# Performance work log

Hardware: AMD Instinct MI355X
Metric: run time of the kernel (lower is better)

## Reference

```python
import jax, jax.numpy as jnp
import numpy as np

L = 248      # max_clip_seq_len
WIN = 3      # window_size
H = 8        # attention heads
D = 768      # input/output dim
HID = 256    # rope hidden dim
SIGMA = 2.0
EPS_LN = 1e-5


def _layernorm(x, g, b):
    m = jnp.mean(x, axis=-1, keepdims=True)
    v = jnp.var(x, axis=-1, keepdims=True)
    return (x - m) / jnp.sqrt(v + EPS_LN) * g + b


def _normalize(x):
    n = jnp.linalg.norm(x, axis=-1, keepdims=True)
    return x / jnp.maximum(n, 1e-12)


def _peb_forward(word_feat, text_feat_full, word_pos, ctx_W, ctx_b, in_W, in_b,
                 out_W, out_b, cn_g, cn_b, r1_W, r1_b, ln_g, ln_b, r2_W, r2_b,
                 pos_emb, pos_temp):
    B, N, _ = word_feat.shape
    valid = word_pos != -1                              # [B,N] bool
    vf = valid.astype(word_feat.dtype)[..., None]       # [B,N,1]
    wp = jnp.clip(word_pos, 0, L - 1)                   # [B,N]
    half = WIN // 2
    offs = jnp.arange(-half, half + 1)
    positions = jnp.clip(wp[..., None] + offs[None, None, :], 0, L - 1)
    ctx = text_feat_full[jnp.arange(B)[:, None, None], positions]
    ctx_anchor = (ctx.reshape(B, N, WIN * D) @ ctx_W + ctx_b) * vf       # [B,N,D]
    q = word_feat * vf                                  # word_proj is Identity (768->768)
    # MultiheadAttention (batch_first), query=q, key=value=ctx_anchor
    hd = D // H
    qp = (q @ in_W[:, :D] + in_b[:D]).reshape(B, N, H, hd)
    kp = (ctx_anchor @ in_W[:, D:2 * D] + in_b[D:2 * D]).reshape(B, N, H, hd)
    vp = (ctx_anchor @ in_W[:, 2 * D:] + in_b[2 * D:]).reshape(B, N, H, hd)
    scores = jnp.einsum('bqhd,bkhd->bhqk', qp, kp) / jnp.sqrt(jnp.asarray(hd, q.dtype))
    attn = jax.nn.softmax(scores, axis=-1)
    ao = jnp.einsum('bhqk,bkhd->bqhd', attn, vp).reshape(B, N, D)
    attn_out = ao @ out_W + out_b
    x = _layernorm(q + attn_out, cn_g, cn_b) * vf       # word_feat_with_ctx
    # rope_mapping: Linear -> GELU -> LayerNorm -> Linear
    rope = _layernorm(jax.nn.gelu(x @ r1_W + r1_b, approximate=False), ln_g, ln_b) @ r2_W + r2_b
    rope_n = _normalize(rope)
    clip_ref_n = _normalize(pos_emb)                    # [L,D]
    temp = jnp.maximum(pos_temp, 0.001)
    logits = jnp.einsum('bnd,ld->bnl', rope_n, clip_ref_n) / temp
    log_q = jax.nn.log_softmax(logits, axis=-1)
    # gaussian soft target over L positions
    pos_idx = jnp.arange(L, dtype=jnp.float32)
    d2 = (pos_idx[None, None, :] - wp[..., None].astype(jnp.float32)) ** 2
    targ = jnp.exp(-d2 / (2.0 * SIGMA ** 2))
    targ = targ / (targ.sum(axis=-1, keepdims=True) + 1e-12)
    lqv = log_q * vf
    tv = targ * vf
    n_valid = valid.sum().astype(jnp.float32)
    safe_t = jnp.where(tv > 0, tv, 1.0)
    kl = jnp.sum(jnp.where(tv > 0, tv * (jnp.log(safe_t) - lqv), 0.0)) / (n_valid + 1e-12)
    # relative position loss on cosine similarity
    pos_sim01 = (jnp.einsum('bnd,bmd->bnm', rope_n, rope_n) + 1.0) / 2.0
    wpf = wp.astype(jnp.float32)
    target_sim = 1.0 - jnp.abs(wpf[:, :, None] - wpf[:, None, :]) / float(L)
    vm2 = vf[:, :, 0][:, None, :] * vf[:, :, 0][:, :, None]
    rel = jnp.sum((pos_sim01 * vm2 - target_sim * vm2) ** 2) / (vm2.sum() + 1e-12)
    peb_loss = (1.0 * kl + 0.5 * rel) * 1.0             # kl_weight=1, rel_weight=0.5, peb_weight=1
    # scatter blended positional features to 248-length sequence (vectorized over batch)
    vals = 0.8 * pos_emb[wp] + 0.2 * rope               # [B,N,D]
    pos_s = jnp.where(valid, wp, L)                     # invalid -> OOB index, dropped
    emb = jnp.zeros((B, L, D), word_feat.dtype).at[jnp.arange(B)[:, None], pos_s].set(vals, mode='drop')
    return emb, peb_loss, kl, rel


def setup_inputs() -> dict:
    key = jax.random.key(0)
    ks = jax.random.split(key, 20)
    B, N = 128, 128
    word_feat = jax.random.normal(ks[0], (B, N, D), jnp.float32)
    text_feat_full = jax.random.normal(ks[1], (B, L, D), jnp.float32)
    # unique sorted positions per batch (scatter is then deterministic, matching torch)
    perms = jax.vmap(lambda k: jax.random.permutation(k, L))(jax.random.split(ks[2], B))
    word_pos = jnp.sort(perms[:, :N], axis=-1).astype(jnp.int32)
    s = 0.02
    return {
        'word_feat': word_feat,
        'text_feat_full': text_feat_full,
        'word_pos': word_pos,
        'ctx_W': s * jax.random.normal(ks[3], (WIN * D, D), jnp.float32),
        'ctx_b': s * jax.random.normal(ks[4], (D,), jnp.float32),
        'in_W': s * jax.random.normal(ks[5], (D, 3 * D), jnp.float32),
        'in_b': s * jax.random.normal(ks[6], (3 * D,), jnp.float32),
        'out_W': s * jax.random.normal(ks[7], (D, D), jnp.float32),
        'out_b': s * jax.random.normal(ks[8], (D,), jnp.float32),
        'cn_g': jnp.ones((D,), jnp.float32) + s * jax.random.normal(ks[9], (D,), jnp.float32),
        'cn_b': s * jax.random.normal(ks[10], (D,), jnp.float32),
        'r1_W': s * jax.random.normal(ks[11], (D, HID), jnp.float32),
        'r1_b': s * jax.random.normal(ks[12], (HID,), jnp.float32),
        'ln_g': jnp.ones((HID,), jnp.float32) + s * jax.random.normal(ks[13], (HID,), jnp.float32),
        'ln_b': s * jax.random.normal(ks[14], (HID,), jnp.float32),
        'r2_W': s * jax.random.normal(ks[15], (HID, D), jnp.float32),
        'r2_b': s * jax.random.normal(ks[16], (D,), jnp.float32),
        'pos_emb': jax.random.normal(ks[17], (L, D), jnp.float32),
        'pos_temp': jnp.asarray(1.0, jnp.float32),
    }


def reference(word_feat, text_feat_full, word_pos, ctx_W, ctx_b, in_W, in_b,
              out_W, out_b, cn_g, cn_b, r1_W, r1_b, ln_g, ln_b, r2_W, r2_b,
              pos_emb, pos_temp):
    return _peb_forward(word_feat, text_feat_full, word_pos, ctx_W, ctx_b, in_W, in_b,
                        out_W, out_b, cn_g, cn_b, r1_W, r1_b, ln_g, ln_b, r2_W, r2_b,
                        pos_emb, pos_temp)
```

## Files before the change

kernel.cpp:

```cpp
#include <hip/hip_runtime.h>
#include <math.h>

#define BB   128
#define NN   128
#define LL   248
#define DD   768
#define HH   8
#define HDh  96
#define HIDN 256
#define MROWS (BB*NN)
#define MB_   (1u<<20)
#define KVLD 1536

typedef unsigned short u16;
typedef unsigned int   u32;
typedef __attribute__((ext_vector_type(8))) short s16x8;
typedef __attribute__((ext_vector_type(4))) float f32x4;

__device__ __forceinline__ u16 f2bf(float x) {
    u32 u = __float_as_uint(x);
    u32 r = u + 0x7fffu + ((u >> 16) & 1u);
    return (u16)(r >> 16);
}
__device__ __forceinline__ float bf2f(u16 h) {
    return __uint_as_float(((u32)h) << 16);
}
__device__ __forceinline__ void gload16(const void* g, void* l) {
    __builtin_amdgcn_global_load_lds(
        (const __attribute__((address_space(1))) void*)g,
        (__attribute__((address_space(3))) void*)l, 16, 0, 0);
}

template<int NT>
__device__ __forceinline__ float breduce_sum(float v, float* red) {
    const int tid = threadIdx.x;
    red[tid] = v; __syncthreads();
#pragma unroll
    for (int o = NT / 2; o > 0; o >>= 1) {
        if (tid < o) red[tid] += red[tid + o];
        __syncthreads();
    }
    float r = red[0]; __syncthreads();
    return r;
}
__device__ __forceinline__ double breduce_sum_d256(double v, double* red) {
    const int tid = threadIdx.x;
    red[tid] = v; __syncthreads();
#pragma unroll
    for (int o = 128; o > 0; o >>= 1) {
        if (tid < o) red[tid] += red[tid + o];
        __syncthreads();
    }
    double r = red[0]; __syncthreads();
    return r;
}

#define TEXT_F4 (BB*LL*DD/4)
#define Q_F4    (MROWS*(DD/4))
__global__ __launch_bounds__(256)
void prep_all_kernel(const float* __restrict__ ctx_W, u16* __restrict__ ctx_Wt,
                     const float* __restrict__ in_W,  u16* __restrict__ in_Wt,
                     const float* __restrict__ out_W, u16* __restrict__ out_Wt,
                     const float* __restrict__ r1_W,  u16* __restrict__ r1_Wt,
                     const float* __restrict__ r2_W,  u16* __restrict__ r2_Wt,
                     const float* __restrict__ text,  u16* __restrict__ textb,
                     const float* __restrict__ wf,    u16* __restrict__ qb,
                     const int* __restrict__ wpos,    int* __restrict__ cpos,
                     const float* __restrict__ pe,    u16* __restrict__ clipb,
                     float* __restrict__ zbias) {
    __shared__ float smem[32 * 33];
    int bid = blockIdx.x;
    const int tid = threadIdx.x;

    if (bid < 4416) {
        const float* src; u16* dst; int C;
        if (bid < 1728)      { src = ctx_W; dst = ctx_Wt; C = 768;  }
        else if (bid < 3456) { src = in_W;  dst = in_Wt;  C = 2304; bid -= 1728; }
        else if (bid < 4032) { src = out_W; dst = out_Wt; C = 768;  bid -= 3456; }
        else if (bid < 4224) { src = r1_W;  dst = r1_Wt;  C = 256;  bid -= 4032; }
        else                 { src = r2_W;  dst = r2_Wt;  C = 768;  bid -= 4224; }
        const int R = (C == 768) ? ((dst == ctx_Wt) ? 2304 : ((dst == out_Wt) ? 768 : 256))
                                 : 768;
        const int ct = C >> 5;
        const int r0 = (bid / ct) * 32, c0 = (bid % ct) * 32;
        const int tx = tid & 31, ty = tid >> 5;
#pragma unroll
        for (int i = 0; i < 32; i += 8)
            smem[(ty + i) * 33 + tx] = src[(size_t)(r0 + ty + i) * C + c0 + tx];
        __syncthreads();
#pragma unroll
        for (int i = 0; i < 32; i += 8)
            dst[(size_t)(c0 + ty + i) * R + r0 + tx] = f2bf(smem[tx * 33 + ty + i]);
    } else if (bid < 4672) {
        const int l = bid - 4416;
        if (l >= LL) {
            for (int j = 0; j < 3; ++j) clipb[(size_t)l * DD + tid + j * 256] = 0;
            return;
        }
        float t[3]; float q = 0.f;
#pragma unroll
        for (int j = 0; j < 3; ++j) {
            t[j] = pe[(size_t)l * DD + tid + j * 256];
            q = fmaf(t[j], t[j], q);
        }
        q = breduce_sum<256>(q, smem);
        float inv = 1.f / fmaxf(sqrtf(q), 1e-12f);
#pragma unroll
        for (int j = 0; j < 3; ++j)
            clipb[(size_t)l * DD + tid + j * 256] = f2bf(t[j] * inv);
    } else {
        const int ebid = bid - 4672;
        if (ebid == 0) {
            for (int r = tid; r < MROWS; r += 256) {
                int w = wpos[r];
                cpos[r] = w < 0 ? 0 : (w > LL - 1 ? LL - 1 : w);
            }
            if (tid < 256) zbias[tid] = 0.f;
        }
        const int lane = tid & 63;
        const int wid = ebid * 4 + (tid >> 6);
        const int NCHUNK = (TEXT_F4 + Q_F4) / 512;
        for (int c = wid; c < NCHUNK; c += 8192) {
            const int base = c * 512;
            if (base < TEXT_F4) {
                const float4* sp = (const float4*)text;
                uint2* op = (uint2*)textb;
                float4 v[8];
#pragma unroll
                for (int j = 0; j < 8; ++j)
                    v[j] = sp[(size_t)base + j * 64 + lane];
#pragma unroll
                for (int j = 0; j < 8; ++j) {
                    uint2 o;
                    o.x = (u32)f2bf(v[j].x) | ((u32)f2bf(v[j].y) << 16);
                    o.y = (u32)f2bf(v[j].z) | ((u32)f2bf(v[j].w) << 16);
                    op[(size_t)base + j * 64 + lane] = o;
                }
            } else {
                const int qb4 = base - TEXT_F4;
                const float4* sp = (const float4*)wf;
                uint2* op = (uint2*)qb;
                float4 v[8]; float vfm[8];
#pragma unroll
                for (int j = 0; j < 8; ++j)
                    v[j] = sp[(size_t)qb4 + j * 64 + lane];
#pragma unroll
                for (int j = 0; j < 8; ++j)
                    vfm[j] = (wpos[(qb4 + j * 64 + lane) / 192] != -1) ? 1.f : 0.f;
#pragma unroll
                for (int j = 0; j < 8; ++j) {
                    uint2 o;
                    o.x = (u32)f2bf(v[j].x * vfm[j]) | ((u32)f2bf(v[j].y * vfm[j]) << 16);
                    o.y = (u32)f2bf(v[j].z * vfm[j]) | ((u32)f2bf(v[j].w * vfm[j]) << 16);
                    op[(size_t)qb4 + j * 64 + lane] = o;
                }
            }
        }
    }
}

template<int GATHER, int CBF16, int MASK>
__device__ __forceinline__ void gemm_tile(
    const int m0, const int n0,
    const u16* __restrict__ A,
    const u16* __restrict__ TXT,
    const int* __restrict__ cpos,
    const u16* __restrict__ Bt,
    const float* __restrict__ bias,
    void* __restrict__ Cout, int ldc, int K,
    const int* __restrict__ wpos,
    u16* Alds, u16* Blds) {
    const int tid = threadIdx.x;
    const int l = tid & 63, wv = tid >> 6;

    const int rw = wv * 8 + (l >> 3);
    const int ce = ((l & 7) ^ (l >> 3)) << 3;

    const int wm = (wv >> 1) * 64, wn = (wv & 1) * 64;
    const int la = l & 15, lg = l >> 4;

    int aoff[4], boff[4];
#pragma unroll
    for (int m = 0; m < 4; ++m) {
        int ra = wm + m * 16 + la;
        aoff[m] = ra * 64 + (((lg ^ (la & 7)) << 3));
        int rb = wn + m * 16 + la;
        boff[m] = rb * 64 + (((lg ^ (la & 7)) << 3));
    }

    const u16* pb[4];
#pragma unroll
    for (int i = 0; i < 4; ++i)
        pb[i] = Bt + (size_t)(n0 + rw + i * 32) * K + ce;

    const u16* pa[4];
    const u16* paw0[4]; const u16* paw1[4]; const u16* paw2[4];
    if constexpr (GATHER) {
#pragma unroll
        for (int i = 0; i < 4; ++i) {
            int g = m0 + rw + i * 32;
            int gb = g >> 7, gc = cpos[g];
            int p0 = gc - 1; p0 = p0 < 0 ? 0 : p0;
            int p1 = gc;
            int p2 = gc + 1; p2 = p2 > LL - 1 ? LL - 1 : p2;
            paw0[i] = TXT + ((size_t)(gb * LL + p0)) * DD + ce;
            paw1[i] = TXT + ((size_t)(gb * LL + p1)) * DD + ce;
            paw2[i] = TXT + ((size_t)(gb * LL + p2)) * DD + ce;
        }
    } else {
#pragma unroll
        for (int i = 0; i < 4; ++i)
            pa[i] = A + (size_t)(m0 + rw + i * 32) * K + ce;
    }

    auto STAGE = [&](int buf, int kt) {
        u16* Ad = Alds + buf * 8192 + wv * 512;
        u16* Bd = Blds + buf * 8192 + wv * 512;
        if constexpr (GATHER) {
            const int w = (kt >= 24) ? 2 : ((kt >= 12) ? 1 : 0);
            const int kin = kt - w * 12;
#pragma unroll
            for (int i = 0; i < 4; ++i) {
                const u16* ai = (w == 0) ? paw0[i] : ((w == 1) ? paw1[i] : paw2[i]);
                gload16(ai + kin * 64, Ad + i * 2048);
            }
        } else {
#pragma unroll
            for (int i = 0; i < 4; ++i)
                gload16(pa[i] + kt * 64, Ad + i * 2048);
        }
#pragma unroll
        for (int i = 0; i < 4; ++i)
            gload16(pb[i] + kt * 64, Bd + i * 2048);
    };

    f32x4 acc[4][4] = {};
    const int nk = GATHER ? 36 : (K >> 6);

    STAGE(0, 0);
    __syncthreads();
#pragma unroll 1
    for (int kt = 0; kt < nk; ++kt) {
        const int cur = kt & 1;
        if (kt + 1 < nk) STAGE(cur ^ 1, kt + 1);
        const int cb = cur * 8192;
#pragma unroll
        for (int kk = 0; kk < 2; ++kk) {
            const int kx = kk << 5;
            s16x8 af[4], bf[4];
#pragma unroll
            for (int m = 0; m < 4; ++m) af[m] = *(const s16x8*)(Alds + cb + (aoff[m] ^ kx));
#pragma unroll
            for (int n = 0; n < 4; ++n) bf[n] = *(const s16x8*)(Blds + cb + (boff[n] ^ kx));
#pragma unroll
            for (int m = 0; m < 4; ++m)
#pragma unroll
                for (int n = 0; n < 4; ++n)
                    acc[m][n] = __builtin_amdgcn_mfma_f32_16x16x32_bf16(
                        af[m], bf[n], acc[m][n], 0, 0, 0);
        }
        __syncthreads();
    }

#pragma unroll
    for (int m = 0; m < 4; ++m) {
        const int rb = m0 + wm + m * 16 + lg * 4;
        float vf[4];
        if constexpr (MASK) {
#pragma unroll
            for (int r = 0; r < 4; ++r) vf[r] = (wpos[rb + r] != -1) ? 1.f : 0.f;
        }
#pragma unroll
        for (int n = 0; n < 4; ++n) {
            const int col = n0 + wn + n * 16 + la;
            const float bv = bias[col];
#pragma unroll
            for (int r = 0; r < 4; ++r) {
                float o = acc[m][n][r] + bv;
                if constexpr (MASK) o *= vf[r];
                if constexpr (CBF16)
                    ((u16*)Cout)[(size_t)(rb + r) * ldc + col] = f2bf(o);
                else
                    ((float*)Cout)[(size_t)(rb + r) * ldc + col] = o;
            }
        }
    }
}

template<int GATHER, int CBF16, int MASK>
__global__ __launch_bounds__(256)
void gemm_bt(const u16* __restrict__ A,
             const u16* __restrict__ TXT,
             const int* __restrict__ cpos,
             const u16* __restrict__ Bt,
             const float* __restrict__ bias,
             void* __restrict__ Cout, int ldc, int K,
             const int* __restrict__ wpos) {
    __shared__ __align__(16) u16 AB[4 * 128 * 64];
    const int gx  = gridDim.x;
    const int hw  = blockIdx.y * gx + blockIdx.x;
    const int nwg = gx * gridDim.y;
    const int cpx = nwg >> 3;
    const int lin = (hw & 7) * cpx + (hw >> 3);
    const int m0 = (lin / gx) * 128, n0 = (lin % gx) * 128;
    gemm_tile<GATHER, CBF16, MASK>(m0, n0, A, TXT, cpos, Bt, bias,
                                   Cout, ldc, K, wpos, AB, AB + 2 * 8192);
}

__global__ __launch_bounds__(256)
void gemm_ctx_qp_kernel(const u16* __restrict__ textb, const int* __restrict__ cpos,
                        const u16* __restrict__ ctx_Wt, const float* __restrict__ ctx_b,
                        u16* __restrict__ ctxa,
                        const u16* __restrict__ qb, const u16* __restrict__ in_Wt,
                        const float* __restrict__ in_b, u16* __restrict__ qpb,
                        const int* __restrict__ wpos) {
    __shared__ __align__(16) u16 AB[4 * 128 * 64];
    const int bid = blockIdx.x;
    if (bid < 768) {
        const int lin = (bid & 7) * 96 + (bid >> 3);
        const int m0 = (lin / 6) * 128, n0 = (lin % 6) * 128;
        gemm_tile<1, 1, 1>(m0, n0, nullptr, textb, cpos, ctx_Wt, ctx_b,
                           ctxa, DD, 3 * DD, wpos, AB, AB + 2 * 8192);
    } else {
        const int b2 = bid - 768;
        const int lin = (b2 & 7) * 96 + (b2 >> 3);
        const int m0 = (lin / 6) * 128, n0 = (lin % 6) * 128;
        gemm_tile<0, 1, 0>(m0, n0, qb, nullptr, nullptr, in_Wt, in_b,
                           qpb, DD, DD, nullptr, AB, AB + 2 * 8192);
    }
}

__device__ __forceinline__ void rel_tile(int blk, const u16* __restrict__ rnb,
                                         const int* __restrict__ wpos,
                                         float* __restrict__ rel_part,
                                         float* __restrict__ vm2_part,
                                         u16* T ) {
    float* red = (float*)(T + 4096);
    const int b = blk >> 1, jh = blk & 1;
    const int tid = threadIdx.x;
    const int l = tid & 63, wv = tid >> 6;
    const int la = l & 15, lg = l >> 4;

    const int f0 = wv * 1024 + l * 16;
    const int f1 = f0 + 4096;
    const int rA0 = f0 >> 6, rA1 = f1 >> 6;
    const int ce0 = ((f0 & 63) ^ (((rA0 >> 1) & 3) << 4)) >> 1;
    const int ce1 = ((f1 & 63) ^ (((rA1 >> 1) & 3) << 4)) >> 1;
    const u16* src0 = rnb + ((size_t)(b * NN + rA0)) * DD + ce0;
    const u16* src1 = rnb + ((size_t)(b * NN + rA1)) * DD + ce1;
    u16* dst0 = T + wv * 512;
    u16* dst1 = T + 2048 + wv * 512;

    int aoff[2];
#pragma unroll
    for (int g = 0; g < 2; ++g) {
        int ra = wv * 32 + g * 16 + la;
        aoff[g] = ra * 32 + ((lg * 8) ^ (((ra >> 1) & 3) << 3));
    }
    int boff[4];
#pragma unroll
    for (int nf = 0; nf < 4; ++nf) {
        int rb = jh * 64 + nf * 16 + la;
        boff[nf] = rb * 32 + ((lg * 8) ^ (((rb >> 1) & 3) << 3));
    }

    f32x4 acc[2][4] = {};
    for (int kt = 0; kt < 24; ++kt) {
        gload16(src0 + kt * 32, dst0);
        gload16(src1 + kt * 32, dst1);
        __syncthreads();
        s16x8 a[2], bf_[4];
#pragma unroll
        for (int g = 0; g < 2; ++g) a[g] = *(const s16x8*)(T + aoff[g]);
#pragma unroll
        for (int nf = 0; nf < 4; ++nf) bf_[nf] = *(const s16x8*)(T + boff[nf]);
#pragma unroll
        for (int g = 0; g < 2; ++g)
#pragma unroll
            for (int nf = 0; nf < 4; ++nf)
                acc[g][nf] = __builtin_amdgcn_mfma_f32_16x16x32_bf16(
                    a[g], bf_[nf], acc[g][nf], 0, 0, 0);
        __syncthreads();
    }

    float csum = 0.f, msum = 0.f;
#pragma unroll
    for (int g = 0; g < 2; ++g) {
        float wif[4], vi[4];
#pragma unroll
        for (int r = 0; r < 4; ++r) {
            int wi = wpos[b * NN + wv * 32 + g * 16 + lg * 4 + r];
            vi[r] = (wi != -1) ? 1.f : 0.f;
            wif[r] = (float)(wi < 0 ? 0 : (wi > LL - 1 ? LL - 1 : wi));
        }
#pragma unroll
        for (int nf = 0; nf < 4; ++nf) {
            int wj = wpos[b * NN + jh * 64 + nf * 16 + la];
            float vj = (wj != -1) ? 1.f : 0.f;
            float wjf = (float)(wj < 0 ? 0 : (wj > LL - 1 ? LL - 1 : wj));
#pragma unroll
            for (int r = 0; r < 4; ++r) {
                float sim = (acc[g][nf][r] + 1.f) * 0.5f;
                float ts  = 1.f - fabsf(wif[r] - wjf) * (1.f / (float)LL);
                float m2  = vi[r] * vj;
                float df  = m2 * (sim - ts);
                csum += df * df;
                msum += m2;
            }
        }
    }
    csum = breduce_sum<256>(csum, red);
    msum = breduce_sum<256>(msum, red);
    if (tid == 0) { rel_part[blk] = csum; vm2_part[blk] = msum; }
}

__global__ __launch_bounds__(256)
void logits_rel_kernel(const u16* __restrict__ rnb, const u16* __restrict__ clipb,
                       const float* __restrict__ zbias, float* __restrict__ logits,
                       const int* __restrict__ wpos,
                       float* __restrict__ relp, float* __restrict__ vmp) {
    __shared__ __align__(16) u16 pool[4 * 128 * 64];
    const int bid = blockIdx.x;
    if (bid < 256) {
        const int lin = (bid & 7) * 32 + (bid >> 3);
        const int m0 = (lin >> 1) * 128, n0 = (lin & 1) * 128;
        gemm_tile<0, 0, 0>(m0, n0, rnb, nullptr, nullptr, clipb, zbias,
                           logits, 256, DD, nullptr, pool, pool + 2 * 8192);
    } else {
        rel_tile(bid - 256, rnb, wpos, relp, vmp, pool);
    }
}

__global__ __launch_bounds__(512)
void attn_mfma_kernel(const u16* __restrict__ qp, const u16* __restrict__ kvb,
                      u16* __restrict__ ao) {
    __shared__ __align__(16) u16 K_lds[128 * 96];
    __shared__ __align__(16) u16 Vt_lds[96 * 128];
    __shared__ __align__(16) u16 P_lds[128 * 128];
    const int bh = blockIdx.x;
    const int b = bh >> 3, h = bh & 7;
    const int tid = threadIdx.x;
    const int l = tid & 63, wv = tid >> 6;
    const int la = l & 15, lg = l >> 4;
    const float scale = 0.10206207261596575f;

    const size_t qbase  = ((size_t)b * NN) * DD + h * HDh;
    const size_t kvbase = ((size_t)b * NN) * KVLD + h * HDh;

#pragma unroll
    for (int i = 0; i < 3; ++i) {
        int f = i * 8192 + wv * 1024 + l * 16;
        int row = f / 192;
        int inner = f - row * 192;
        gload16((const char*)(kvb + kvbase + (size_t)row * KVLD) + inner,
                (char*)K_lds + f);
    }

    uint4 vchunk[3]; int vkey[3], vd0[3];
#pragma unroll
    for (int i = 0; i < 3; ++i) {
        int c = tid + i * 512;
        int key = c / 12, dc = c - key * 12;
        vkey[i] = key; vd0[i] = dc * 8;
        vchunk[i] = *(const uint4*)(kvb + kvbase + (size_t)key * KVLD + DD + dc * 8);
    }

    const int q0 = wv * 16;
    s16x8 qf[3];
#pragma unroll
    for (int kt = 0; kt < 3; ++kt)
        qf[kt] = *(const s16x8*)(qp + qbase + (size_t)(q0 + la) * DD + kt * 32 + lg * 8);

#pragma unroll
    for (int i = 0; i < 3; ++i) {
        const u16* e = (const u16*)&vchunk[i];
#pragma unroll
        for (int j = 0; j < 8; ++j) {
            int d = vd0[i] + j;
            int byte = ((d * 128 + vkey[i]) * 2) ^ ((d & 7) << 4);
            *(u16*)((char*)Vt_lds + byte) = e[j];
        }
    }
    __syncthreads();

    f32x4 sacc[8] = {};
#pragma unroll
    for (int kt = 0; kt < 3; ++kt) {
#pragma unroll
        for (int nf = 0; nf < 8; ++nf) {
            s16x8 bfr = *(const s16x8*)(K_lds + (nf * 16 + la) * 96 + kt * 32 + lg * 8);
            sacc[nf] = __builtin_amdgcn_mfma_f32_16x16x32_bf16(qf[kt], bfr, sacc[nf], 0, 0, 0);
        }
    }

#pragma unroll
    for (int r = 0; r < 4; ++r) {
        float m = -1e30f;
#pragma unroll
        for (int nf = 0; nf < 8; ++nf) m = fmaxf(m, sacc[nf][r]);
#pragma unroll
        for (int o = 8; o > 0; o >>= 1) m = fmaxf(m, __shfl_xor(m, o, 64));
        m *= scale;
        float p[8]; float s = 0.f;
#pragma unroll
        for (int nf = 0; nf < 8; ++nf) { p[nf] = expf(sacc[nf][r] * scale - m); s += p[nf]; }
#pragma unroll
        for (int o = 8; o > 0; o >>= 1) s += __shfl_xor(s, o, 64);
        const float inv = 1.f / s;
        const int q = q0 + lg * 4 + r;
#pragma unroll
        for (int nf = 0; nf < 8; ++nf) {
            int byte = ((q * 128 + nf * 16 + la) * 2) ^ ((q & 7) << 4);
            *(u16*)((char*)P_lds + byte) = f2bf(p[nf] * inv);
        }
    }
    __syncthreads();

    f32x4 oacc[6] = {};
#pragma unroll
    for (int kk = 0; kk < 4; ++kk) {
        const int qrow = q0 + la;
        int abyte = ((qrow * 128 + kk * 32 + lg * 8) * 2) ^ ((qrow & 7) << 4);
        s16x8 af = *(const s16x8*)((char*)P_lds + abyte);
#pragma unroll
        for (int nf = 0; nf < 6; ++nf) {
            const int d = nf * 16 + la;
            int bbyte = ((d * 128 + kk * 32 + lg * 8) * 2) ^ ((d & 7) << 4);
            s16x8 bfr = *(const s16x8*)((char*)Vt_lds + bbyte);
            oacc[nf] = __builtin_amdgcn_mfma_f32_16x16x32_bf16(af, bfr, oacc[nf], 0, 0, 0);
        }
    }

#pragma unroll
    for (int nf = 0; nf < 6; ++nf) {
#pragma unroll
        for (int r = 0; r < 4; ++r) {
            const int q = q0 + lg * 4 + r;
            ao[qbase + (size_t)q * DD + nf * 16 + la] = f2bf(oacc[nf][r]);
        }
    }
}

__global__ __launch_bounds__(256)
void ln768_kernel(const u16* __restrict__ qb, const u16* __restrict__ at,
                  const int* __restrict__ wpos, const float* __restrict__ g,
                  const float* __restrict__ bta, u16* __restrict__ xout) {
    __shared__ float red[256];
    const int r = blockIdx.x, tid = threadIdx.x;
    const float vf = (wpos[r] != -1) ? 1.f : 0.f;
    float t[3]; float s = 0.f, q = 0.f;
#pragma unroll
    for (int j = 0; j < 3; ++j) {
        int d = tid + j * 256;
        t[j] = bf2f(qb[(size_t)r * DD + d]) + bf2f(at[(size_t)r * DD + d]);
        s += t[j];
        q = fmaf(t[j], t[j], q);
    }
    s = breduce_sum<256>(s, red);
    q = breduce_sum<256>(q, red);
    float mean = s * (1.f / DD);
    float var  = q * (1.f / DD) - mean * mean;
    float inv  = 1.f / sqrtf(var + 1e-5f);
#pragma unroll
    for (int j = 0; j < 3; ++j) {
        int d = tid + j * 256;
        xout[(size_t)r * DD + d] = f2bf(((t[j] - mean) * inv * g[d] + bta[d]) * vf);
    }
}

__global__ __launch_bounds__(256)
void ln256_gelu_kernel(const u16* __restrict__ g1, const float* __restrict__ lg,
                       const float* __restrict__ lb, u16* __restrict__ hout) {
    __shared__ float red[256];
    const int r = blockIdx.x, tid = threadIdx.x;
    float v  = bf2f(g1[(size_t)r * HIDN + tid]);
    float ge = 0.5f * v * (1.f + erff(v * 0.7071067811865475f));
    float s = breduce_sum<256>(ge, red);
    float q = breduce_sum<256>(ge * ge, red);
    float mean = s * (1.f / HIDN);
    float var  = q * (1.f / HIDN) - mean * mean;
    float inv  = 1.f / sqrtf(var + 1e-5f);
    hout[(size_t)r * HIDN + tid] = f2bf((ge - mean) * inv * lg[tid] + lb[tid]);
}

__global__ __launch_bounds__(256)
void norm_emb_kernel(const u16* __restrict__ ropeb, const float* __restrict__ pe,
                     const int* __restrict__ wpos, u16* __restrict__ rnb,
                     float* __restrict__ emb) {
    __shared__ float red[256];
    const int bid = blockIdx.x;
    const int tid = threadIdx.x;
    if (bid < MROWS) {
        const int r = bid;
        float t[3]; float q = 0.f;
#pragma unroll
        for (int j = 0; j < 3; ++j) {
            t[j] = bf2f(ropeb[(size_t)r * DD + tid + j * 256]);
            q = fmaf(t[j], t[j], q);
        }
        q = breduce_sum<256>(q, red);
        float inv = 1.f / fmaxf(sqrtf(q), 1e-12f);
#pragma unroll
        for (int j = 0; j < 3; ++j)
            rnb[(size_t)r * DD + tid + j * 256] = f2bf(t[j] * inv);
    } else {
        const int bl = bid - MROWS;
        const int b = bl / LL, l = bl - b * LL;
        const int* wp = wpos + b * NN;
        int lo = 0, hi = NN - 1, found = -1;
        while (lo <= hi) {
            int mid = (lo + hi) >> 1;
            int v = wp[mid];
            if (v == l) { found = mid; break; }
            if (v < l) lo = mid + 1; else hi = mid - 1;
        }
        float* dst = emb + (size_t)bl * DD;
        if (found >= 0) {
            const u16* rr = ropeb + (size_t)(b * NN + found) * DD;
#pragma unroll
            for (int j = 0; j < 3; ++j) {
                int d = tid + j * 256;
                dst[d] = 0.8f * pe[(size_t)l * DD + d] + 0.2f * bf2f(rr[d]);
            }
        } else {
#pragma unroll
            for (int j = 0; j < 3; ++j)
                dst[tid + j * 256] = 0.f;
        }
    }
}

__global__ __launch_bounds__(256)
void kl_lite_kernel(const float* __restrict__ logits, const int* __restrict__ wpos,
                    const float* __restrict__ pos_temp, float* __restrict__ klp) {
    const int row = blockIdx.x * 4 + (threadIdx.x >> 6);
    const int l = threadIdx.x & 63;
    const float invt = 1.f / fmaxf(pos_temp[0], 0.001f);
    const float* lrow = logits + (size_t)row * 256;

    float lg[4];
#pragma unroll
    for (int q = 0; q < 4; ++q) {
        int c = l + q * 64;
        lg[q] = (c < LL) ? lrow[c] * invt : -1e30f;
    }
    float m = fmaxf(fmaxf(lg[0], lg[1]), fmaxf(lg[2], lg[3]));
#pragma unroll
    for (int o = 32; o > 0; o >>= 1) m = fmaxf(m, __shfl_xor(m, o, 64));

    float S = 0.f;
#pragma unroll
    for (int q = 0; q < 4; ++q) S += expf(lg[q] - m);
#pragma unroll
    for (int o = 32; o > 0; o >>= 1) S += __shfl_xor(S, o, 64);
    const float logZ = m + logf(S);

    const int wr = wpos[row];
    const bool valid = (wr != -1);
    const int wp = wr < 0 ? 0 : (wr > LL - 1 ? LL - 1 : wr);

    float targ[4]; float tsum = 0.f;
#pragma unroll
    for (int q = 0; q < 4; ++q) {
        int c = l + q * 64;
        float dl = (float)c - (float)wp;
        targ[q] = (c < LL) ? expf(-dl * dl * 0.125f) : 0.f;
        tsum += targ[q];
    }
#pragma unroll
    for (int o = 32; o > 0; o >>= 1) tsum += __shfl_xor(tsum, o, 64);
    const float tden = 1.f / (tsum + 1e-12f);

    float c_ = 0.f;
#pragma unroll
    for (int q = 0; q < 4; ++q) {
        float tn = targ[q] * tden;
        if (valid && tn > 0.f) c_ += tn * (logf(tn) - (lg[q] - logZ));
    }
#pragma unroll
    for (int o = 32; o > 0; o >>= 1) c_ += __shfl_xor(c_, o, 64);
    if (l == 0) klp[row] = c_;
}

__global__ __launch_bounds__(256)
void final_kernel(const float* __restrict__ klp, const float* __restrict__ relp,
                  const float* __restrict__ vmp, const int* __restrict__ wpos,
                  float* __restrict__ outs) {
    __shared__ double rd[256];
    const int tid = threadIdx.x;
    double kl = 0.0, rel = 0.0, vm = 0.0, nv = 0.0;
    for (int r = tid; r < MROWS; r += 256) {
        kl += (double)klp[r];
        nv += (wpos[r] != -1) ? 1.0 : 0.0;
    }
    if (tid < 256) {
        rel += (double)relp[tid];
        vm  += (double)vmp[tid];
    }
    kl  = breduce_sum_d256(kl, rd);
    rel = breduce_sum_d256(rel, rd);
    vm  = breduce_sum_d256(vm, rd);
    nv  = breduce_sum_d256(nv, rd);
    if (tid == 0) {
        float klf  = (float)(kl / (nv + 1e-12));
        float relf = (float)(rel / (vm + 1e-12));
        outs[0] = klf + 0.5f * relf;
        outs[1] = klf;
        outs[2] = relf;
    }
}

extern "C" void kernel_launch(void* const* d_in, const int* in_sizes, int n_in,
                              void* d_out, int out_size, void* d_ws, size_t ws_size,
                              hipStream_t stream) {
    (void)in_sizes; (void)n_in; (void)ws_size; (void)out_size;

    const float* word_feat = (const float*)d_in[0];
    const float* text      = (const float*)d_in[1];
    const int*   wpos      = (const int*)d_in[2];
    const float* ctx_W     = (const float*)d_in[3];
    const float* ctx_b     = (const float*)d_in[4];
    const float* in_W      = (const float*)d_in[5];
    const float* in_b      = (const float*)d_in[6];
    const float* out_W     = (const float*)d_in[7];
    const float* out_b     = (const float*)d_in[8];
    const float* cn_g      = (const float*)d_in[9];
    const float* cn_b      = (const float*)d_in[10];
    const float* r1_W      = (const float*)d_in[11];
    const float* r1_b      = (const float*)d_in[12];
    const float* ln_g      = (const float*)d_in[13];
    const float* ln_b      = (const float*)d_in[14];
    const float* r2_W      = (const float*)d_in[15];
    const float* r2_b      = (const float*)d_in[16];
    const float* pos_emb   = (const float*)d_in[17];
    const float* pos_temp  = (const float*)d_in[18];

    char* W = (char*)d_ws;
    u16*   ctx_Wt = (u16*)(W);
    u16*   in_Wt  = ctx_Wt + (size_t)768 * 2304;
    u16*   out_Wt = in_Wt  + (size_t)2304 * 768;
    u16*   r1_Wt  = out_Wt + (size_t)768 * 768;
    u16*   r2_Wt  = r1_Wt  + (size_t)256 * 768;
    u16*   clipb  = r2_Wt + (size_t)768 * 256;
    int*   cposb  = (int*)(clipb + (size_t)256 * DD);
    float* klp    = (float*)(cposb + MROWS);
    float* relp   = klp + MROWS;
    float* vmp    = relp + 256;
    float* zbias  = vmp + 256;
    u16*   textb  = (u16*)(W + (size_t)12 * MB_);
    u16*   atoutb = textb;
    float* logits = (float*)(W + (size_t)12 * MB_);
    u16*   xb     = (u16*)(W + (size_t)36 * MB_);
    u16*   qb     = (u16*)(W + (size_t)60 * MB_);
    u16*   ctxa   = (u16*)(W + (size_t)86 * MB_);
    u16*   aob    = ctxa;
    u16*   rnb    = ctxa;
    u16*   qpb    = (u16*)(W + (size_t)112 * MB_);
    u16*   g1b    = (u16*)(W + (size_t)112 * MB_);
    u16*   hb     = (u16*)(W + (size_t)128 * MB_);
    u16*   kvb    = (u16*)(W + (size_t)138 * MB_);
    u16*   ropeb  = kvb;

    dim3 blk(256);

    prep_all_kernel<<<dim3(4416 + 256 + 2048), blk, 0, stream>>>(
        ctx_W, ctx_Wt, in_W, in_Wt, out_W, out_Wt, r1_W, r1_Wt, r2_W, r2_Wt,
        text, textb, word_feat, qb, wpos, cposb, pos_emb, clipb, zbias);

    dim3 g768(6, 128);
    dim3 g1536(12, 128);

    gemm_ctx_qp_kernel<<<dim3(1536), blk, 0, stream>>>(
        textb, cposb, ctx_Wt, ctx_b, ctxa, qb, in_Wt, in_b, qpb, wpos);
    gemm_bt<0, 1, 0><<<g1536, blk, 0, stream>>>(
        ctxa, nullptr, nullptr, in_Wt + (size_t)768 * 768, in_b + DD, kvb, KVLD, DD, nullptr);
    attn_mfma_kernel<<<dim3(BB * HH), dim3(512), 0, stream>>>(qpb, kvb, aob);
    gemm_bt<0, 1, 0><<<g768, blk, 0, stream>>>(
        aob, nullptr, nullptr, out_Wt, out_b, atoutb, DD, DD, nullptr);
    ln768_kernel<<<dim3(MROWS), blk, 0, stream>>>(qb, atoutb, wpos, cn_g, cn_b, xb);
    gemm_bt<0, 1, 0><<<dim3(2, 128), blk, 0, stream>>>(
        xb, nullptr, nullptr, r1_Wt, r1_b, g1b, HIDN, DD, nullptr);
    ln256_gelu_kernel<<<dim3(MROWS), blk, 0, stream>>>(g1b, ln_g, ln_b, hb);
    gemm_bt<0, 1, 0><<<g768, blk, 0, stream>>>(
        hb, nullptr, nullptr, r2_Wt, r2_b, ropeb, DD, HIDN, nullptr);
    norm_emb_kernel<<<dim3(MROWS + BB * LL), blk, 0, stream>>>(
        ropeb, pos_emb, wpos, rnb, (float*)d_out);
    logits_rel_kernel<<<dim3(512), blk, 0, stream>>>(
        rnb, clipb, zbias, logits, wpos, relp, vmp);
    kl_lite_kernel<<<dim3(MROWS / 4), blk, 0, stream>>>(logits, wpos, pos_temp, klp);
    final_kernel<<<dim3(1), blk, 0, stream>>>(
        klp, relp, vmp, wpos, (float*)d_out + (size_t)BB * LL * DD);
}
```

Baseline: 400.7 us.

## Switch GEMM tile to K=32 triple-buffered LDS pipeline with one barrier per step

The shared GEMM tile moves from K=64 double-buffered staging to K=32 tiles in a three-slot ring with a prefetch distance of two. Explicit vmcnt waits and a single s_barrier per iteration replace the two syncthreads per step, and the LDS swizzle is changed to match the 32-wide rows. The aim is to hide more global-load latency and cut barrier stalls, and the smaller LDS footprint may allow higher occupancy. In exchange there are twice as many loop iterations, each with half the MFMA work. The rel_tile code that shares the pool still fits in the reduced buffer.

```diff
diff --git a/kernel.cpp b/kernel.cpp
--- a/kernel.cpp
+++ b/kernel.cpp
@@ -173,8 +173,11 @@
     const int tid = threadIdx.x;
     const int l = tid & 63, wv = tid >> 6;
 
-    const int rw = wv * 8 + (l >> 3);
-    const int ce = ((l & 7) ^ (l >> 3)) << 3;
+    const int f0 = wv * 1024 + l * 16;
+    const int f1 = f0 + 4096;
+    const int rA0 = f0 >> 6, rA1 = f1 >> 6;
+    const int c0e = ((f0 & 63) ^ (((rA0 >> 1) & 3) << 4)) >> 1;
+    const int c1e = ((f1 & 63) ^ (((rA1 >> 1) & 3) << 4)) >> 1;
 
     const int wm = (wv >> 1) * 64, wn = (wv & 1) * 64;
     const int la = l & 15, lg = l >> 4;
@@ -183,84 +186,84 @@
 #pragma unroll
     for (int m = 0; m < 4; ++m) {
         int ra = wm + m * 16 + la;
-        aoff[m] = ra * 64 + (((lg ^ (la & 7)) << 3));
+        aoff[m] = ra * 32 + ((lg * 8) ^ (((ra >> 1) & 3) << 3));
         int rb = wn + m * 16 + la;
-        boff[m] = rb * 64 + (((lg ^ (la & 7)) << 3));
-    }
-
-    const u16* pb[4];
-#pragma unroll
-    for (int i = 0; i < 4; ++i)
-        pb[i] = Bt + (size_t)(n0 + rw + i * 32) * K + ce;
-
-    const u16* pa[4];
-    const u16* paw0[4]; const u16* paw1[4]; const u16* paw2[4];
+        boff[m] = rb * 32 + ((lg * 8) ^ (((rb >> 1) & 3) << 3));
+    }
+
+    const u16* pb0 = Bt + (size_t)(n0 + rA0) * K + c0e;
+    const u16* pb1 = Bt + (size_t)(n0 + rA1) * K + c1e;
+
+    const u16* pa0 = nullptr; const u16* pa1 = nullptr;
+    const u16* paw0[3]; const u16* paw1[3];
     if constexpr (GATHER) {
-#pragma unroll
-        for (int i = 0; i < 4; ++i) {
-            int g = m0 + rw + i * 32;
-            int gb = g >> 7, gc = cpos[g];
-            int p0 = gc - 1; p0 = p0 < 0 ? 0 : p0;
-            int p1 = gc;
-            int p2 = gc + 1; p2 = p2 > LL - 1 ? LL - 1 : p2;
-            paw0[i] = TXT + ((size_t)(gb * LL + p0)) * DD + ce;
-            paw1[i] = TXT + ((size_t)(gb * LL + p1)) * DD + ce;
-            paw2[i] = TXT + ((size_t)(gb * LL + p2)) * DD + ce;
+        int g0 = m0 + rA0, g1 = m0 + rA1;
+        int gb0 = g0 >> 7, gb1 = g1 >> 7;
+        int gc0 = cpos[g0], gc1 = cpos[g1];
+#pragma unroll
+        for (int w = 0; w < 3; ++w) {
+            int p0 = gc0 + w - 1; p0 = p0 < 0 ? 0 : (p0 > LL - 1 ? LL - 1 : p0);
+            int p1 = gc1 + w - 1; p1 = p1 < 0 ? 0 : (p1 > LL - 1 ? LL - 1 : p1);
+            paw0[w] = TXT + ((size_t)(gb0 * LL + p0)) * DD + c0e;
+            paw1[w] = TXT + ((size_t)(gb1 * LL + p1)) * DD + c1e;
         }
     } else {
-#pragma unroll
-        for (int i = 0; i < 4; ++i)
-            pa[i] = A + (size_t)(m0 + rw + i * 32) * K + ce;
+        pa0 = A + (size_t)(m0 + rA0) * K + c0e;
+        pa1 = A + (size_t)(m0 + rA1) * K + c1e;
     }
 
     auto STAGE = [&](int buf, int kt) {
-        u16* Ad = Alds + buf * 8192 + wv * 512;
-        u16* Bd = Blds + buf * 8192 + wv * 512;
+        u16* Ad = Alds + buf * 4096 + wv * 512;
+        u16* Bd = Blds + buf * 4096 + wv * 512;
+        const u16 *ga0, *ga1;
         if constexpr (GATHER) {
-            const int w = (kt >= 24) ? 2 : ((kt >= 12) ? 1 : 0);
-            const int kin = kt - w * 12;
-#pragma unroll
-            for (int i = 0; i < 4; ++i) {
-                const u16* ai = (w == 0) ? paw0[i] : ((w == 1) ? paw1[i] : paw2[i]);
-                gload16(ai + kin * 64, Ad + i * 2048);
-            }
+            const int w = (kt >= 48) ? 2 : ((kt >= 24) ? 1 : 0);
+            const int kin = kt - w * 24;
+            ga0 = paw0[w] + kin * 32;
+            ga1 = paw1[w] + kin * 32;
         } else {
-#pragma unroll
-            for (int i = 0; i < 4; ++i)
-                gload16(pa[i] + kt * 64, Ad + i * 2048);
-        }
-#pragma unroll
-        for (int i = 0; i < 4; ++i)
-            gload16(pb[i] + kt * 64, Bd + i * 2048);
+            ga0 = pa0 + kt * 32;
+            ga1 = pa1 + kt * 32;
+        }
+        gload16(ga0, Ad);
+        gload16(ga1, Ad + 2048);
+        gload16(pb0 + kt * 32, Bd);
+        gload16(pb1 + kt * 32, Bd + 2048);
     };
 
     f32x4 acc[4][4] = {};
-    const int nk = GATHER ? 36 : (K >> 6);
+    const int nk = K >> 5;
 
     STAGE(0, 0);
-    __syncthreads();
+    STAGE(1, 1);
 #pragma unroll 1
     for (int kt = 0; kt < nk; ++kt) {
-        const int cur = kt & 1;
-        if (kt + 1 < nk) STAGE(cur ^ 1, kt + 1);
-        const int cb = cur * 8192;
-#pragma unroll
-        for (int kk = 0; kk < 2; ++kk) {
-            const int kx = kk << 5;
-            s16x8 af[4], bf[4];
-#pragma unroll
-            for (int m = 0; m < 4; ++m) af[m] = *(const s16x8*)(Alds + cb + (aoff[m] ^ kx));
-#pragma unroll
-            for (int n = 0; n < 4; ++n) bf[n] = *(const s16x8*)(Blds + cb + (boff[n] ^ kx));
-#pragma unroll
-            for (int m = 0; m < 4; ++m)
-#pragma unroll
-                for (int n = 0; n < 4; ++n)
-                    acc[m][n] = __builtin_amdgcn_mfma_f32_16x16x32_bf16(
-                        af[m], bf[n], acc[m][n], 0, 0, 0);
-        }
-        __syncthreads();
-    }
+        if (kt + 1 < nk) {
+            asm volatile("s_waitcnt vmcnt(4)" ::: "memory");
+        } else {
+            asm volatile("s_waitcnt vmcnt(0)" ::: "memory");
+        }
+        __builtin_amdgcn_sched_barrier(0);
+        __builtin_amdgcn_s_barrier();
+        __builtin_amdgcn_sched_barrier(0);
+        if (kt + 2 < nk) {
+            int bn = kt + 2;
+            STAGE(bn - (bn / 3) * 3, bn);
+        }
+        const int cb = (kt - (kt / 3) * 3) * 4096;
+        s16x8 af[4], bf[4];
+#pragma unroll
+        for (int m = 0; m < 4; ++m) af[m] = *(const s16x8*)(Alds + cb + aoff[m]);
+#pragma unroll
+        for (int n = 0; n < 4; ++n) bf[n] = *(const s16x8*)(Blds + cb + boff[n]);
+#pragma unroll
+        for (int m = 0; m < 4; ++m)
+#pragma unroll
+            for (int n = 0; n < 4; ++n)
+                acc[m][n] = __builtin_amdgcn_mfma_f32_16x16x32_bf16(
+                    af[m], bf[n], acc[m][n], 0, 0, 0);
+    }
+    __syncthreads();
 
 #pragma unroll
     for (int m = 0; m < 4; ++m) {
@@ -296,7 +299,7 @@
              const float* __restrict__ bias,
              void* __restrict__ Cout, int ldc, int K,
              const int* __restrict__ wpos) {
-    __shared__ __align__(16) u16 AB[4 * 128 * 64];
+    __shared__ __align__(16) u16 AB[2 * 3 * 128 * 32];
     const int gx  = gridDim.x;
     const int hw  = blockIdx.y * gx + blockIdx.x;
     const int nwg = gx * gridDim.y;
@@ -304,7 +307,7 @@
     const int lin = (hw & 7) * cpx + (hw >> 3);
     const int m0 = (lin / gx) * 128, n0 = (lin % gx) * 128;
     gemm_tile<GATHER, CBF16, MASK>(m0, n0, A, TXT, cpos, Bt, bias,
-                                   Cout, ldc, K, wpos, AB, AB + 2 * 8192);
+                                   Cout, ldc, K, wpos, AB, AB + 3 * 4096);
 }
 
 __global__ __launch_bounds__(256)
@@ -314,19 +317,19 @@
                         const u16* __restrict__ qb, const u16* __restrict__ in_Wt,
                         const float* __restrict__ in_b, u16* __restrict__ qpb,
                         const int* __restrict__ wpos) {
-    __shared__ __align__(16) u16 AB[4 * 128 * 64];
+    __shared__ __align__(16) u16 AB[2 * 3 * 128 * 32];
     const int bid = blockIdx.x;
     if (bid < 768) {
         const int lin = (bid & 7) * 96 + (bid >> 3);
         const int m0 = (lin / 6) * 128, n0 = (lin % 6) * 128;
         gemm_tile<1, 1, 1>(m0, n0, nullptr, textb, cpos, ctx_Wt, ctx_b,
-                           ctxa, DD, 3 * DD, wpos, AB, AB + 2 * 8192);
+                           ctxa, DD, 3 * DD, wpos, AB, AB + 3 * 4096);
     } else {
         const int b2 = bid - 768;
         const int lin = (b2 & 7) * 96 + (b2 >> 3);
         const int m0 = (lin / 6) * 128, n0 = (lin % 6) * 128;
         gemm_tile<0, 1, 0>(m0, n0, qb, nullptr, nullptr, in_Wt, in_b,
-                           qpb, DD, DD, nullptr, AB, AB + 2 * 8192);
+                           qpb, DD, DD, nullptr, AB, AB + 3 * 4096);
     }
 }
 
@@ -419,13 +422,13 @@
                        const float* __restrict__ zbias, float* __restrict__ logits,
                        const int* __restrict__ wpos,
                        float* __restrict__ relp, float* __restrict__ vmp) {
-    __shared__ __align__(16) u16 pool[4 * 128 * 64];
+    __shared__ __align__(16) u16 pool[2 * 3 * 128 * 32];
     const int bid = blockIdx.x;
     if (bid < 256) {
         const int lin = (bid & 7) * 32 + (bid >> 3);
         const int m0 = (lin >> 1) * 128, n0 = (lin & 1) * 128;
         gemm_tile<0, 0, 0>(m0, n0, rnb, nullptr, nullptr, clipb, zbias,
-                           logits, 256, DD, nullptr, pool, pool + 2 * 8192);
+                           logits, 256, DD, nullptr, pool, pool + 3 * 4096);
     } else {
         rel_tile(bid - 256, rnb, wpos, relp, vmp, pool);
     }
```

Result: slower. 416.0 us (+3.8%).
